# Performance work log

Hardware: AMD Instinct MI355X
Metric: run time of the kernel (lower is better)

## Reference

```python
import jax, jax.numpy as jnp
import numpy as np


def _gru_layer(x, w_ih, w_hh, b_ih, b_hh):
    """PyTorch-semantics GRU over x:[B,T,I]. w_ih:[3H,I], w_hh:[3H,H]."""
    B, T, I = x.shape
    H = w_hh.shape[1]
    # precompute input-side gates for all timesteps: [T,B,3H]
    gx = (jnp.einsum('bti,gi->btg', x, w_ih) + b_ih).transpose(1, 0, 2)

    def step(h, gx_t):
        gh = h @ w_hh.T + b_hh  # [B,3H]
        xr, xz, xn = jnp.split(gx_t, 3, axis=-1)
        hr, hz, hn = jnp.split(gh, 3, axis=-1)
        r = jax.nn.sigmoid(xr + hr)
        z = jax.nn.sigmoid(xz + hz)
        n = jnp.tanh(xn + r * hn)
        h_new = (1.0 - z) * n + z * h
        return h_new, h_new

    h0 = jnp.zeros((B, H), dtype=x.dtype)
    _, hs = jax.lax.scan(step, h0, gx)  # hs: [T,B,H]
    return hs.transpose(1, 0, 2)


def _gru_params(key, in_size, hidden):
    k = 1.0 / np.sqrt(hidden)
    k1, k2, k3, k4 = jax.random.split(key, 4)
    w_ih = jax.random.uniform(k1, (3 * hidden, in_size), minval=-k, maxval=k, dtype=jnp.float32)
    w_hh = jax.random.uniform(k2, (3 * hidden, hidden), minval=-k, maxval=k, dtype=jnp.float32)
    b_ih = jax.random.uniform(k3, (3 * hidden,), minval=-k, maxval=k, dtype=jnp.float32)
    b_hh = jax.random.uniform(k4, (3 * hidden,), minval=-k, maxval=k, dtype=jnp.float32)
    return w_ih, w_hh, b_ih, b_hh


def setup_inputs() -> dict:
    key = jax.random.key(0)
    ks = jax.random.split(key, 6)
    B, T = 256, 1024
    x = jax.random.normal(ks[0], (B, T), dtype=jnp.float32)
    sizes = [(1, 256), (256, 128), (128, 128), (128, 256)]
    d = {'x': x}
    for i, (isz, h) in enumerate(sizes):
        w_ih, w_hh, b_ih, b_hh = _gru_params(ks[1 + i], isz, h)
        d[f'w_ih{i+1}'] = w_ih
        d[f'w_hh{i+1}'] = w_hh
        d[f'b_ih{i+1}'] = b_ih
        d[f'b_hh{i+1}'] = b_hh
    kw, kb = jax.random.split(ks[5])
    kk = 1.0 / np.sqrt(256.0)
    d['w_out'] = jax.random.uniform(kw, (1, 256), minval=-kk, maxval=kk, dtype=jnp.float32)
    d['b_out'] = jax.random.uniform(kb, (1,), minval=-kk, maxval=kk, dtype=jnp.float32)
    return d


def reference(x, w_ih1, w_hh1, b_ih1, b_hh1,
              w_ih2, w_hh2, b_ih2, b_hh2,
              w_ih3, w_hh3, b_ih3, b_hh3,
              w_ih4, w_hh4, b_ih4, b_hh4,
              w_out, b_out):
    h = x[..., None]  # [B,T,1]
    h = _gru_layer(h, w_ih1, w_hh1, b_ih1, b_hh1)
    h = _gru_layer(h, w_ih2, w_hh2, b_ih2, b_hh2)
    h = _gru_layer(h, w_ih3, w_hh3, b_ih3, b_hh3)
    h = _gru_layer(h, w_ih4, w_hh4, b_ih4, b_hh4)
    y = jnp.einsum('bth,oh->bto', h, w_out) + b_out  # TimeDistributed Linear(256,1)
    return y.reshape(y.shape[0], -1)  # flatten from dim 1 -> [B,T]
```

## Files before the change

### kernel.cpp

```cpp
#include <hip/hip_runtime.h>
#include <math.h>


__device__ __forceinline__ float sigmoidf_(float v) {
    return 1.0f / (1.0f + __expf(-v));
}
__device__ __forceinline__ float tanhf_(float v) {
    float e = __expf(2.0f * v);
    return 1.0f - 2.0f / (e + 1.0f);
}

__global__ void prep_k(const float* __restrict__ src, float* __restrict__ dst,
                       int H, int J) {
    int idx = blockIdx.x * 256 + threadIdx.x;
    int total = 3 * H * J;
    if (idx < total) {
        int g = idx / (H * J);
        int rem = idx - g * H * J;
        int u = rem / J;
        int j = rem - u * J;
        dst[(u * 3 + g) * J + j] = src[(g * H + u) * J + j];
    }
}


__device__ __forceinline__ void flag_st(int* p, int v) {
    __hip_atomic_store(p, v, __ATOMIC_RELAXED, __HIP_MEMORY_SCOPE_AGENT);
}
__device__ __forceinline__ int flag_ld(const int* p) {
    return __hip_atomic_load(p, __ATOMIC_RELAXED, __HIP_MEMORY_SCOPE_AGENT);
}
__device__ __forceinline__ void ex_store(float* p, float v) {
    __hip_atomic_store(p, v, __ATOMIC_RELAXED, __HIP_MEMORY_SCOPE_AGENT);
}

__device__ __forceinline__ void pollwait(const int* p, int tgt, bool active,
                                         int& fc) {
    if (threadIdx.x < 64) {
        bool need = active && (fc < tgt);
        if (__any(need)) {
            int spins = 0;
            while (true) {
                if (need) { fc = flag_ld(p); need = (fc < tgt); }
                if (!__any(need)) break;
                if (++spins > 200000) break;
                __builtin_amdgcn_s_sleep(1);
            }
        }
    }
    __syncthreads();
}


template <int J>
__device__ __forceinline__ void stageW(float* dst, const float* src) {
    constexpr int NF4 = J / 32;
    const int lane = threadIdx.x & 63;
    float4 tmp[NF4];
    #pragma unroll
    for (int k = 0; k < NF4; ++k) {
        const float* p = src + (size_t)(k * 64 + lane) * 4;
        asm volatile("global_load_dwordx4 %0, %1, off sc0 sc1"
                     : "=v"(tmp[k]) : "v"(p) : "memory");
    }
    asm volatile("s_waitcnt vmcnt(0)" ::: "memory");
    #pragma unroll
    for (int k = 0; k < NF4; ++k)
        *(float4*)(dst + (k * 64 + lane) * 4) = tmp[k];
}

template <int J>
__device__ __forceinline__ void zeroW(float* dst) {
    const int lane = threadIdx.x & 63;
    #pragma unroll
    for (int k = 0; k < J / 32; ++k)
        *(float4*)(dst + (k * 64 + lane) * 4) = make_float4(0.f, 0.f, 0.f, 0.f);
}

template <int U, int J>
__device__ __forceinline__ void ring_store(float* hout, const float* hst) {
    constexpr int LU = (U == 32) ? 5 : 4;
    #pragma unroll
    for (int k = 0; k < (32 * U) / 256; ++k) {
        int i = k * 256 + threadIdx.x;
        int b = i >> LU;
        int c = i & (U - 1);
        ex_store(hout + b * J + c, hst[b * (U + 4) + c]);
    }
}


template <int J, int WST>
__device__ __forceinline__ void dotA4(const float* __restrict__ wb,
                                      const float* __restrict__ hb, int kl,
                                      float (&a)[8][12]) {
    #pragma unroll 2
    for (int it = 0; it < J / 32; ++it) {
        const int j = (it * 8 + kl) * 4;
        float4 h4[8];
        #pragma unroll
        for (int b = 0; b < 8; ++b)
            h4[b] = *(const float4*)(hb + b * J + j);
        #pragma unroll
        for (int i = 0; i < 4; ++i) {
            #pragma unroll
            for (int ch = 0; ch < 3; ++ch) {
                float4 w = *(const float4*)(wb + i * WST + ch * J + j);
                #pragma unroll
                for (int b8 = 0; b8 < 8; ++b8) {
                    float& acc = a[i * 2 + (b8 >> 2)][ch * 4 + (b8 & 3)];
                    acc = fmaf(w.x, h4[b8].x, acc);
                    acc = fmaf(w.y, h4[b8].y, acc);
                    acc = fmaf(w.z, h4[b8].z, acc);
                    acc = fmaf(w.w, h4[b8].w, acc);
                }
            }
        }
    }
}

template <int J, int WST>
__device__ __forceinline__ void dotB2(const float* __restrict__ wb,
                                      const float* __restrict__ hb, int kl,
                                      float (&a)[8][6]) {
    #pragma unroll 2
    for (int it = 0; it < J / 32; ++it) {
        const int j = (it * 8 + kl) * 4;
        float4 h4[8];
        #pragma unroll
        for (int b = 0; b < 8; ++b)
            h4[b] = *(const float4*)(hb + b * J + j);
        #pragma unroll
        for (int i = 0; i < 2; ++i) {
            #pragma unroll
            for (int ch = 0; ch < 3; ++ch) {
                float4 w = *(const float4*)(wb + i * WST + ch * J + j);
                #pragma unroll
                for (int b8 = 0; b8 < 8; ++b8) {
                    float& acc = a[i * 4 + (b8 >> 1)][ch * 2 + (b8 & 1)];
                    acc = fmaf(w.x, h4[b8].x, acc);
                    acc = fmaf(w.y, h4[b8].y, acc);
                    acc = fmaf(w.z, h4[b8].z, acc);
                    acc = fmaf(w.w, h4[b8].w, acc);
                }
            }
        }
    }
}

template <int G, int F>
__device__ __forceinline__ void rscat(float (&a)[G][F], int kl) {
    #pragma unroll
    for (int lev = 0; (1 << lev) < G; ++lev) {
        const int m = 1 << lev;
        const int g = G >> (lev + 1);
        const bool hi = ((kl >> lev) & 1) != 0;
        #pragma unroll
        for (int gg = 0; gg < g; ++gg) {
            #pragma unroll
            for (int f = 0; f < F; ++f) {
                float give = hi ? a[gg][f] : a[gg + g][f];
                float got = __shfl_xor(give, m, 64);
                a[gg][f] = (hi ? a[gg + g][f] : a[gg][f]) + got;
            }
        }
    }
}

__global__ __launch_bounds__(256) void gru_pipe_kernel(
    const float* __restrict__ x,
    const float* __restrict__ w_ih1,
    const float* __restrict__ b_ih1, const float* __restrict__ b_hh1,
    const float* __restrict__ b_ih2, const float* __restrict__ b_hh2,
    const float* __restrict__ b_ih3, const float* __restrict__ b_hh3,
    const float* __restrict__ b_ih4, const float* __restrict__ b_hh4,
    const float* __restrict__ wA_hh1,
    const float* __restrict__ wA_ih2,
    const float* __restrict__ wA_hh2,
    const float* __restrict__ wA_ih3,
    const float* __restrict__ wA_hh3,
    const float* __restrict__ wA_ih4,
    const float* __restrict__ wA_hh4,
    const float* __restrict__ w_out, const float* __restrict__ b_out,
    int* __restrict__ flags,
    float* __restrict__ ex,
    float* __restrict__ out)
{
    const int tid = threadIdx.x;
    const int lane = tid & 63;
    const int w = tid >> 6;
    const int usl = lane >> 3;
    const int kl = lane & 7;
    const int gf = ((kl & 1) << 2) | (kl & 2) | ((kl >> 2) & 1);
    extern __shared__ float smem[];
    __shared__ float xs[32];

    const int bg = blockIdx.x & 7;
    const int rest = blockIdx.x >> 3;
    const int s = rest >> 3;
    const int us = rest & 7;

    int* fb = flags + bg * 128;
    int* arr_own = fb + s * 32;

    const int* pT = arr_own; int dT = -1000000000; bool aT = false;
    const int* pM = arr_own; bool aM = false;
    if (tid < 8) {
        if (s > 0) { pT = fb + (s - 1) * 32 + tid; dT = 1; aT = true; }
        pM = arr_own + tid; aM = true;
    } else if (tid < 16) {
        if (s < 3) { pT = fb + (s + 1) * 32 + (tid - 8); dT = -3; aT = true; }
    }
    int fcT = 0, fcM = 0;

    float* exb = ex + (size_t)bg * 98304;
    float* h1r = exb;
    float* h2r = exb + 32768;
    float* h3r = exb + 49152;
    float* h4r = exb + 65536;

    if (s == 0) {
        float* wlds = smem;
        float* hprev = smem + 24704;
        float* hst = smem + 32896;
        {
            const float* srcw = wA_hh1 + (size_t)us * 32 * 768;
            for (int i = tid; i < 24576; i += 256) {
                int uu = i / 768, r = i - uu * 768;
                wlds[uu * 772 + r] = srcw[i];
            }
        }
        __syncthreads();
        const int u_sl = usl * 4 + (gf >> 1);
        const int bhi = gf & 1;
        const int u = us * 32 + u_sl;
        const float* wbh = wlds + usl * 4 * 772;
        const float* hbh = hprev + w * 2048;
        const float br = b_ih1[u] + b_hh1[u];
        const float bz = b_ih1[u + 256] + b_hh1[u + 256];
        const float bxn = b_ih1[u + 512];
        const float bhn = b_hh1[u + 512];
        const float wir = w_ih1[u], wiz = w_ih1[u + 256], win = w_ih1[u + 512];
        for (int t = 0; t < 1024; ++t) {
            pollwait(pT, t + dT, aT, fcT);
            if (tid < 32) xs[tid] = x[(size_t)(bg * 32 + tid) * 1024 + t];
            pollwait(pM, t, aM, fcM);
            if (t > 0) stageW<256>(hprev + w * 2048,
                                   h1r + (size_t)((t - 1) & 3) * 8192 + w * 2048);
            else       zeroW<256>(hprev + w * 2048);
            float ah[8][12] = {};
            dotA4<256, 772>(wbh, hbh, kl, ah);
            rscat<8, 12>(ah, kl);
            float* hout = h1r + (size_t)(t & 3) * 8192;
            #pragma unroll
            for (int bl = 0; bl < 4; ++bl) {
                int b32 = w * 8 + bhi * 4 + bl;
                float xv = xs[b32];
                float rr = sigmoidf_(ah[0][bl] + br + xv * wir);
                float zz = sigmoidf_(ah[0][4 + bl] + bz + xv * wiz);
                float nn = tanhf_(xv * win + bxn + rr * (ah[0][8 + bl] + bhn));
                float hp = hprev[b32 * 256 + u];
                hst[b32 * 36 + u_sl] = (1.f - zz) * nn + zz * hp;
            }
            __syncthreads();
            ring_store<32, 256>(hout + us * 32, hst);
            asm volatile("s_waitcnt vmcnt(0)" ::: "memory");
            __syncthreads();
            if (tid == 0) flag_st(arr_own + us, t + 1);
        }
    } else if (s == 1) {
        float* wlds = smem;
        float* hin = smem + 6208;
        float* hprev = smem + 14400;
        float* hst = smem + 18496;
        {
            const float* srcw = wA_hh2 + (size_t)us * 16 * 384;
            for (int i = tid; i < 6144; i += 256) {
                int uu = i / 384, r = i - uu * 384;
                wlds[uu * 388 + r] = srcw[i];
            }
        }
        __syncthreads();
        const int u_sl = usl * 2 + (gf >> 2);
        const int bq = gf & 3;
        const int u = us * 16 + u_sl;
        const float* wbh = wlds + usl * 2 * 388;
        const float* wbi = wA_ih2 + (size_t)(us * 16 + usl * 2) * 768;
        const float* hbi = hin + w * 2048;
        const float* hbh = hprev + w * 1024;
        const float br = b_ih2[u] + b_hh2[u];
        const float bz = b_ih2[u + 128] + b_hh2[u + 128];
        const float bxn = b_ih2[u + 256];
        const float bhn = b_hh2[u + 256];
        for (int t = 0; t < 1024; ++t) {
            pollwait(pT, t + dT, aT, fcT);
            stageW<256>(hin + w * 2048, h1r + (size_t)(t & 3) * 8192 + w * 2048);
            float ai[8][6] = {};
            dotB2<256, 768>(wbi, hbi, kl, ai);
            rscat<8, 6>(ai, kl);
            pollwait(pM, t, aM, fcM);
            if (t > 0) stageW<128>(hprev + w * 1024,
                                   h2r + (size_t)((t - 1) & 3) * 4096 + w * 1024);
            else       zeroW<128>(hprev + w * 1024);
            float ah[8][6] = {};
            dotB2<128, 388>(wbh, hbh, kl, ah);
            rscat<8, 6>(ah, kl);
            float* hout = h2r + (size_t)(t & 3) * 4096;
            #pragma unroll
            for (int bl = 0; bl < 2; ++bl) {
                int b32 = w * 8 + bq * 2 + bl;
                float rr = sigmoidf_(ai[0][bl] + ah[0][bl] + br);
                float zz = sigmoidf_(ai[0][2 + bl] + ah[0][2 + bl] + bz);
                float nn = tanhf_(ai[0][4 + bl] + bxn + rr * (ah[0][4 + bl] + bhn));
                float hp = hprev[b32 * 128 + u];
                hst[b32 * 20 + u_sl] = (1.f - zz) * nn + zz * hp;
            }
            __syncthreads();
            ring_store<16, 128>(hout + us * 16, hst);
            asm volatile("s_waitcnt vmcnt(0)" ::: "memory");
            __syncthreads();
            if (tid == 0) flag_st(arr_own + us, t + 1);
        }
    } else if (s == 2) {
        float* wlds = smem;
        float* hin = smem + 6208;
        float* hprev = smem + 10304;
        float* hst = smem + 14400;
        {
            const float* srcw = wA_hh3 + (size_t)us * 16 * 384;
            for (int i = tid; i < 6144; i += 256) {
                int uu = i / 384, r = i - uu * 384;
                wlds[uu * 388 + r] = srcw[i];
            }
        }
        __syncthreads();
        const int u_sl = usl * 2 + (gf >> 2);
        const int bq = gf & 3;
        const int u = us * 16 + u_sl;
        const float* wbh = wlds + usl * 2 * 388;
        const float* wbi = wA_ih3 + (size_t)(us * 16 + usl * 2) * 384;
        const float* hbi = hin + w * 1024;
        const float* hbh = hprev + w * 1024;
        const float br = b_ih3[u] + b_hh3[u];
        const float bz = b_ih3[u + 128] + b_hh3[u + 128];
        const float bxn = b_ih3[u + 256];
        const float bhn = b_hh3[u + 256];
        for (int t = 0; t < 1024; ++t) {
            pollwait(pT, t + dT, aT, fcT);
            stageW<128>(hin + w * 1024, h2r + (size_t)(t & 3) * 4096 + w * 1024);
            float ai[8][6] = {};
            dotB2<128, 384>(wbi, hbi, kl, ai);
            rscat<8, 6>(ai, kl);
            pollwait(pM, t, aM, fcM);
            if (t > 0) stageW<128>(hprev + w * 1024,
                                   h3r + (size_t)((t - 1) & 3) * 4096 + w * 1024);
            else       zeroW<128>(hprev + w * 1024);
            float ah[8][6] = {};
            dotB2<128, 388>(wbh, hbh, kl, ah);
            rscat<8, 6>(ah, kl);
            float* hout = h3r + (size_t)(t & 3) * 4096;
            #pragma unroll
            for (int bl = 0; bl < 2; ++bl) {
                int b32 = w * 8 + bq * 2 + bl;
                float rr = sigmoidf_(ai[0][bl] + ah[0][bl] + br);
                float zz = sigmoidf_(ai[0][2 + bl] + ah[0][2 + bl] + bz);
                float nn = tanhf_(ai[0][4 + bl] + bxn + rr * (ah[0][4 + bl] + bhn));
                float hp = hprev[b32 * 128 + u];
                hst[b32 * 20 + u_sl] = (1.f - zz) * nn + zz * hp;
            }
            __syncthreads();
            ring_store<16, 128>(hout + us * 16, hst);
            asm volatile("s_waitcnt vmcnt(0)" ::: "memory");
            __syncthreads();
            if (tid == 0) flag_st(arr_own + us, t + 1);
        }
    } else {
        float* wlds = smem;
        float* hin = smem + 24704;
        float* hprev = smem + 28800;
        float* hst = smem + 36992;
        {
            const float* srcw = wA_hh4 + (size_t)us * 32 * 768;
            for (int i = tid; i < 24576; i += 256) {
                int uu = i / 768, r = i - uu * 768;
                wlds[uu * 772 + r] = srcw[i];
            }
        }
        __syncthreads();
        const int u_sl = usl * 4 + (gf >> 1);
        const int bhi = gf & 1;
        const int u = us * 32 + u_sl;
        const float* wbh = wlds + usl * 4 * 772;
        const float* wbi = wA_ih4 + (size_t)(us * 32 + usl * 4) * 384;
        const float* hbi = hin + w * 1024;
        const float* hbh = hprev + w * 2048;
        const float br = b_ih4[u] + b_hh4[u];
        const float bz = b_ih4[u + 256] + b_hh4[u + 256];
        const float bxn = b_ih4[u + 512];
        const float bhn = b_hh4[u + 512];
        const float wo = w_out[u];
        for (int t = 0; t < 1024; ++t) {
            pollwait(pT, t + dT, aT, fcT);
            stageW<128>(hin + w * 1024, h3r + (size_t)(t & 3) * 4096 + w * 1024);
            float ai[8][12] = {};
            dotA4<128, 384>(wbi, hbi, kl, ai);
            rscat<8, 12>(ai, kl);
            pollwait(pM, t, aM, fcM);
            if (t > 0) stageW<256>(hprev + w * 2048,
                                   h4r + (size_t)((t - 1) & 3) * 8192 + w * 2048);
            else       zeroW<256>(hprev + w * 2048);
            float ah[8][12] = {};
            dotA4<256, 772>(wbh, hbh, kl, ah);
            rscat<8, 12>(ah, kl);
            float* hout = h4r + (size_t)(t & 3) * 8192;
            float pk[4];
            #pragma unroll
            for (int bl = 0; bl < 4; ++bl) {
                int b32 = w * 8 + bhi * 4 + bl;
                float rr = sigmoidf_(ai[0][bl] + ah[0][bl] + br);
                float zz = sigmoidf_(ai[0][4 + bl] + ah[0][4 + bl] + bz);
                float nn = tanhf_(ai[0][8 + bl] + bxn + rr * (ah[0][8 + bl] + bhn));
                float hp = hprev[b32 * 256 + u];
                float hnew = (1.f - zz) * nn + zz * hp;
                hst[b32 * 36 + u_sl] = hnew;
                pk[bl] = wo * hnew;
            }
            #pragma unroll
            for (int bl = 0; bl < 4; ++bl) {
                pk[bl] += __shfl_xor(pk[bl], 1, 64);
                pk[bl] += __shfl_xor(pk[bl], 2, 64);
                pk[bl] += __shfl_xor(pk[bl], 8, 64);
                pk[bl] += __shfl_xor(pk[bl], 16, 64);
                pk[bl] += __shfl_xor(pk[bl], 32, 64);
            }
            __syncthreads();
            ring_store<32, 256>(hout + us * 32, hst);
            asm volatile("s_waitcnt vmcnt(0)" ::: "memory");
            __syncthreads();
            if (tid == 0) flag_st(arr_own + us, t + 1);
            if ((lane & 59) == 0) {
                #pragma unroll
                for (int bl = 0; bl < 4; ++bl) {
                    float v = pk[bl];
                    if (us == 0) v += b_out[0];
                    atomicAdd(out + (size_t)(bg * 32 + w * 8 + bhi * 4 + bl) * 1024 + t, v);
                }
            }
        }
    }
}

extern "C" void kernel_launch(void* const* d_in, const int* in_sizes, int n_in,
                              void* d_out, int out_size, void* d_ws, size_t ws_size,
                              hipStream_t stream) {
    const float* x     = (const float*)d_in[0];
    const float* w_ih1 = (const float*)d_in[1];
    const float* w_hh1 = (const float*)d_in[2];
    const float* b_ih1 = (const float*)d_in[3];
    const float* b_hh1 = (const float*)d_in[4];
    const float* w_ih2 = (const float*)d_in[5];
    const float* w_hh2 = (const float*)d_in[6];
    const float* b_ih2 = (const float*)d_in[7];
    const float* b_hh2 = (const float*)d_in[8];
    const float* w_ih3 = (const float*)d_in[9];
    const float* w_hh3 = (const float*)d_in[10];
    const float* b_ih3 = (const float*)d_in[11];
    const float* b_hh3 = (const float*)d_in[12];
    const float* w_ih4 = (const float*)d_in[13];
    const float* w_hh4 = (const float*)d_in[14];
    const float* b_ih4 = (const float*)d_in[15];
    const float* b_hh4 = (const float*)d_in[16];
    const float* w_out = (const float*)d_in[17];
    const float* b_out = (const float*)d_in[18];

    float* ws = (float*)d_ws;
    float* wA_hh1 = ws;
    float* wA_ih2 = wA_hh1 + 196608;
    float* wA_hh2 = wA_ih2 + 98304;
    float* wA_ih3 = wA_hh2 + 49152;
    float* wA_hh3 = wA_ih3 + 49152;
    float* wA_ih4 = wA_hh3 + 49152;
    float* wA_hh4 = wA_ih4 + 98304;
    float* ex     = wA_hh4 + 196608;
    int*   flags  = (int*)(ex + 786432);

    (void)hipMemsetAsync(flags, 0, 1024 * sizeof(int), stream);
    (void)hipMemsetAsync(d_out, 0, 256 * 1024 * sizeof(float), stream);

    prep_k<<<768, 256, 0, stream>>>(w_hh1, wA_hh1, 256, 256);
    prep_k<<<384, 256, 0, stream>>>(w_ih2, wA_ih2, 128, 256);
    prep_k<<<192, 256, 0, stream>>>(w_hh2, wA_hh2, 128, 128);
    prep_k<<<192, 256, 0, stream>>>(w_ih3, wA_ih3, 128, 128);
    prep_k<<<192, 256, 0, stream>>>(w_hh3, wA_hh3, 128, 128);
    prep_k<<<384, 256, 0, stream>>>(w_ih4, wA_ih4, 256, 128);
    prep_k<<<768, 256, 0, stream>>>(w_hh4, wA_hh4, 256, 256);

    const int dyn_lds = 38144 * (int)sizeof(float);
    (void)hipFuncSetAttribute((const void*)gru_pipe_kernel,
                              hipFuncAttributeMaxDynamicSharedMemorySize, dyn_lds);

    gru_pipe_kernel<<<256, 256, dyn_lds, stream>>>(
        x, w_ih1, b_ih1, b_hh1, b_ih2, b_hh2, b_ih3, b_hh3, b_ih4, b_hh4,
        wA_hh1, wA_ih2, wA_hh2, wA_ih3, wA_hh3, wA_ih4, wA_hh4,
        w_out, b_out, flags, ex, (float*)d_out);
}
```

Before: 19.65 ms.

## Split GRU recurrent dot products across two K-halves with 512-thread blocks

Doubles the block to 512 threads and splits each gate dot product's reduction dimension across two wave groups. The partial sums are merged through LDS with an added khmerge step. Input-side and hidden-side gate sums now share one accumulator, the ih2/ih3 weights are staged into LDS, and h is stored directly to the exchange ring instead of via an LDS transpose. The aim is to shorten the per-timestep serial critical path, at the cost of extra __syncthreads and LDS traffic per step and roughly double the register-pressure constraints under launch_bounds(512).

```diff
diff --git a/kernel.cpp b/kernel.cpp
--- a/kernel.cpp
+++ b/kernel.cpp
@@ -53,7 +53,7 @@
 
 
 template <int J>
-__device__ __forceinline__ void stageW(float* dst, const float* src) {
+__device__ __forceinline__ void stage8(float* dst, const float* src) {
     constexpr int NF4 = J / 32;
     const int lane = threadIdx.x & 63;
     float4 tmp[NF4];
@@ -70,90 +70,77 @@
 }
 
 template <int J>
-__device__ __forceinline__ void zeroW(float* dst) {
+__device__ __forceinline__ void zero8(float* dst) {
     const int lane = threadIdx.x & 63;
     #pragma unroll
     for (int k = 0; k < J / 32; ++k)
         *(float4*)(dst + (k * 64 + lane) * 4) = make_float4(0.f, 0.f, 0.f, 0.f);
 }
 
-template <int U, int J>
-__device__ __forceinline__ void ring_store(float* hout, const float* hst) {
-    constexpr int LU = (U == 32) ? 5 : 4;
+template <int J, int WST, int NCH3, int F>
+__device__ __forceinline__ void dotA(const float* __restrict__ wb,
+                                     const float* __restrict__ hb,
+                                     int kh, int kl, float (&a)[8][F]) {
     #pragma unroll
-    for (int k = 0; k < (32 * U) / 256; ++k) {
-        int i = k * 256 + threadIdx.x;
-        int b = i >> LU;
-        int c = i & (U - 1);
-        ex_store(hout + b * J + c, hst[b * (U + 4) + c]);
-    }
-}
-
-
-template <int J, int WST>
-__device__ __forceinline__ void dotA4(const float* __restrict__ wb,
-                                      const float* __restrict__ hb, int kl,
-                                      float (&a)[8][12]) {
-    #pragma unroll 2
-    for (int it = 0; it < J / 32; ++it) {
-        const int j = (it * 8 + kl) * 4;
+    for (int itl = 0; itl < J / 64; ++itl) {
+        const int j = ((kh * (J / 64) + itl) * 8 + kl) * 4;
         float4 h4[8];
         #pragma unroll
-        for (int b = 0; b < 8; ++b)
-            h4[b] = *(const float4*)(hb + b * J + j);
+        for (int b = 0; b < 8; ++b) h4[b] = *(const float4*)(hb + b * J + j);
         #pragma unroll
         for (int i = 0; i < 4; ++i) {
             #pragma unroll
             for (int ch = 0; ch < 3; ++ch) {
-                float4 w = *(const float4*)(wb + i * WST + ch * J + j);
-                #pragma unroll
-                for (int b8 = 0; b8 < 8; ++b8) {
-                    float& acc = a[i * 2 + (b8 >> 2)][ch * 4 + (b8 & 3)];
-                    acc = fmaf(w.x, h4[b8].x, acc);
-                    acc = fmaf(w.y, h4[b8].y, acc);
-                    acc = fmaf(w.z, h4[b8].z, acc);
-                    acc = fmaf(w.w, h4[b8].w, acc);
-                }
-            }
-        }
-    }
-}
-
-template <int J, int WST>
-__device__ __forceinline__ void dotB2(const float* __restrict__ wb,
-                                      const float* __restrict__ hb, int kl,
-                                      float (&a)[8][6]) {
-    #pragma unroll 2
-    for (int it = 0; it < J / 32; ++it) {
-        const int j = (it * 8 + kl) * 4;
+                float4 wv = *(const float4*)(wb + i * 8 * WST + ch * J + j);
+                const int fb = (ch < 2 ? ch : NCH3) * 4;
+                #pragma unroll
+                for (int b = 0; b < 8; ++b) {
+                    float& acc = a[i * 2 + (b >> 2)][fb + (b & 3)];
+                    acc = fmaf(wv.x, h4[b].x, acc);
+                    acc = fmaf(wv.y, h4[b].y, acc);
+                    acc = fmaf(wv.z, h4[b].z, acc);
+                    acc = fmaf(wv.w, h4[b].w, acc);
+                }
+            }
+        }
+    }
+}
+
+template <int J, int WST, int NCH3>
+__device__ __forceinline__ void dotB(const float* __restrict__ wb,
+                                     const float* __restrict__ hb,
+                                     int kh, int kl, float (&a)[8][8]) {
+    #pragma unroll
+    for (int itl = 0; itl < J / 64; ++itl) {
+        const int j = ((kh * (J / 64) + itl) * 8 + kl) * 4;
         float4 h4[8];
         #pragma unroll
-        for (int b = 0; b < 8; ++b)
-            h4[b] = *(const float4*)(hb + b * J + j);
+        for (int b = 0; b < 8; ++b) h4[b] = *(const float4*)(hb + b * J + j);
         #pragma unroll
         for (int i = 0; i < 2; ++i) {
             #pragma unroll
             for (int ch = 0; ch < 3; ++ch) {
-                float4 w = *(const float4*)(wb + i * WST + ch * J + j);
-                #pragma unroll
-                for (int b8 = 0; b8 < 8; ++b8) {
-                    float& acc = a[i * 4 + (b8 >> 1)][ch * 2 + (b8 & 1)];
-                    acc = fmaf(w.x, h4[b8].x, acc);
-                    acc = fmaf(w.y, h4[b8].y, acc);
-                    acc = fmaf(w.z, h4[b8].z, acc);
-                    acc = fmaf(w.w, h4[b8].w, acc);
-                }
-            }
-        }
-    }
-}
-
-template <int G, int F>
-__device__ __forceinline__ void rscat(float (&a)[G][F], int kl) {
+                float4 wv = *(const float4*)(wb + i * 8 * WST + ch * J + j);
+                const int fb = (ch < 2 ? ch : NCH3) * 2;
+                #pragma unroll
+                for (int b = 0; b < 8; ++b) {
+                    float& acc = a[i * 4 + (b >> 1)][fb + (b & 1)];
+                    acc = fmaf(wv.x, h4[b].x, acc);
+                    acc = fmaf(wv.y, h4[b].y, acc);
+                    acc = fmaf(wv.z, h4[b].z, acc);
+                    acc = fmaf(wv.w, h4[b].w, acc);
+                }
+            }
+        }
+    }
+}
+
+template <int F>
+__device__ __forceinline__ void rscat8(float (&a)[8][F], int kl) {
     #pragma unroll
-    for (int lev = 0; (1 << lev) < G; ++lev) {
+    for (int lev = 0; lev < 3; ++lev) {
         const int m = 1 << lev;
-        const int g = G >> (lev + 1);
+        const int g = 8 >> (lev + 1);
         const bool hi = ((kl >> lev) & 1) != 0;
         #pragma unroll
         for (int gg = 0; gg < g; ++gg) {
@@ -167,7 +154,24 @@
     }
 }
 
-__global__ __launch_bounds__(256) void gru_pipe_kernel(
+template <int F, int F0, int NF>
+__device__ __forceinline__ void khmerge(float* xb, float (&a)[8][F],
+                                        int w, int lane) {
+    if (w >= 4) {
+        #pragma unroll
+        for (int k = 0; k < NF; ++k)
+            xb[((w - 4) * 64 + lane) * 8 + k] = a[0][F0 + k];
+    }
+    __syncthreads();
+    if (w < 4) {
+        #pragma unroll
+        for (int k = 0; k < NF; ++k)
+            a[0][F0 + k] += xb[(w * 64 + lane) * 8 + k];
+    }
+    __syncthreads();
+}
+
+__global__ __launch_bounds__(512) void gru_pipe_kernel(
     const float* __restrict__ x,
     const float* __restrict__ w_ih1,
     const float* __restrict__ b_ih1, const float* __restrict__ b_hh1,
@@ -189,9 +193,10 @@
     const int tid = threadIdx.x;
     const int lane = tid & 63;
     const int w = tid >> 6;
+    const int bh = w & 3;
+    const int kh = w >> 2;
     const int usl = lane >> 3;
     const int kl = lane & 7;
-    const int gf = ((kl & 1) << 2) | (kl & 2) | ((kl >> 2) & 1);
     extern __shared__ float smem[];
     __shared__ float xs[32];
 
@@ -200,16 +205,16 @@
     const int s = rest >> 3;
     const int us = rest & 7;
 
-    int* fb = flags + bg * 128;
-    int* arr_own = fb + s * 32;
+    int* fbp = flags + bg * 128;
+    int* arr_own = fbp + s * 32;
 
     const int* pT = arr_own; int dT = -1000000000; bool aT = false;
     const int* pM = arr_own; bool aM = false;
     if (tid < 8) {
-        if (s > 0) { pT = fb + (s - 1) * 32 + tid; dT = 1; aT = true; }
+        if (s > 0) { pT = fbp + (s - 1) * 32 + tid; dT = 1; aT = true; }
         pM = arr_own + tid; aM = true;
     } else if (tid < 16) {
-        if (s < 3) { pT = fb + (s + 1) * 32 + (tid - 8); dT = -3; aT = true; }
+        if (s < 3) { pT = fbp + (s + 1) * 32 + (tid - 8); dT = -3; aT = true; }
     }
     int fcT = 0, fcM = 0;
 
@@ -222,20 +227,21 @@
     if (s == 0) {
         float* wlds = smem;
         float* hprev = smem + 24704;
-        float* hst = smem + 32896;
+        float* xb = smem + 32896;
         {
             const float* srcw = wA_hh1 + (size_t)us * 32 * 768;
-            for (int i = tid; i < 24576; i += 256) {
+            for (int i = tid; i < 24576; i += 512) {
                 int uu = i / 768, r = i - uu * 768;
                 wlds[uu * 772 + r] = srcw[i];
             }
         }
         __syncthreads();
-        const int u_sl = usl * 4 + (gf >> 1);
-        const int bhi = gf & 1;
-        const int u = us * 32 + u_sl;
-        const float* wbh = wlds + usl * 4 * 772;
-        const float* hbh = hprev + w * 2048;
+        const int iown = ((kl & 1) << 1) | ((kl >> 1) & 1);
+        const int k2 = (kl >> 2) & 1;
+        const int ul = usl + 8 * iown;
+        const int u = us * 32 + ul;
+        const float* wbh = wlds + usl * 772;
+        const float* hbh = hprev + bh * 2048;
         const float br = b_ih1[u] + b_hh1[u];
         const float bz = b_ih1[u + 256] + b_hh1[u + 256];
         const float bxn = b_ih1[u + 512];
@@ -245,131 +251,141 @@
             pollwait(pT, t + dT, aT, fcT);
             if (tid < 32) xs[tid] = x[(size_t)(bg * 32 + tid) * 1024 + t];
             pollwait(pM, t, aM, fcM);
-            if (t > 0) stageW<256>(hprev + w * 2048,
-                                   h1r + (size_t)((t - 1) & 3) * 8192 + w * 2048);
-            else       zeroW<256>(hprev + w * 2048);
-            float ah[8][12] = {};
-            dotA4<256, 772>(wbh, hbh, kl, ah);
-            rscat<8, 12>(ah, kl);
-            float* hout = h1r + (size_t)(t & 3) * 8192;
-            #pragma unroll
-            for (int bl = 0; bl < 4; ++bl) {
-                int b32 = w * 8 + bhi * 4 + bl;
-                float xv = xs[b32];
-                float rr = sigmoidf_(ah[0][bl] + br + xv * wir);
-                float zz = sigmoidf_(ah[0][4 + bl] + bz + xv * wiz);
-                float nn = tanhf_(xv * win + bxn + rr * (ah[0][8 + bl] + bhn));
-                float hp = hprev[b32 * 256 + u];
-                hst[b32 * 36 + u_sl] = (1.f - zz) * nn + zz * hp;
-            }
-            __syncthreads();
-            ring_store<32, 256>(hout + us * 32, hst);
+            if (t > 0) stage8<256>(hprev + bh * 2048,
+                                   h1r + (size_t)((t - 1) & 3) * 8192 + bh * 2048);
+            else       zero8<256>(hprev + bh * 2048);
+            float a[8][12] = {};
+            dotA<256, 772, 2, 12>(wbh, hbh, kh, kl, a);
+            rscat8<12>(a, kl);
+            khmerge<12, 0, 8>(xb, a, w, lane);
+            khmerge<12, 8, 4>(xb, a, w, lane);
+            if (w < 4) {
+                float* hout = h1r + (size_t)(t & 3) * 8192;
+                #pragma unroll
+                for (int bl = 0; bl < 4; ++bl) {
+                    int b32 = bh * 8 + k2 * 4 + bl;
+                    float xv = xs[b32];
+                    float rr = sigmoidf_(a[0][bl] + br + xv * wir);
+                    float zz = sigmoidf_(a[0][4 + bl] + bz + xv * wiz);
+                    float nn = tanhf_(xv * win + bxn + rr * (a[0][8 + bl] + bhn));
+                    float hp = hprev[b32 * 256 + u];
+                    ex_store(hout + b32 * 256 + u, (1.f - zz) * nn + zz * hp);
+                }
+            }
             asm volatile("s_waitcnt vmcnt(0)" ::: "memory");
             __syncthreads();
             if (tid == 0) flag_st(arr_own + us, t + 1);
         }
     } else if (s == 1) {
-        float* wlds = smem;
-        float* hin = smem + 6208;
-        float* hprev = smem + 14400;
-        float* hst = smem + 18496;
+        float* whhL = smem;
+        float* wihL = smem + 6208;
+        float* hin = smem + 18560;
+        float* hprev = smem + 26752;
+        float* xb = smem + 30848;
         {
             const float* srcw = wA_hh2 + (size_t)us * 16 * 384;
-            for (int i = tid; i < 6144; i += 256) {
+            for (int i = tid; i < 6144; i += 512) {
                 int uu = i / 384, r = i - uu * 384;
-                wlds[uu * 388 + r] = srcw[i];
+                whhL[uu * 388 + r] = srcw[i];
+            }
+            const float* srci = wA_ih2 + (size_t)us * 16 * 768;
+            for (int i = tid; i < 12288; i += 512) {
+                int uu = i / 768, r = i - uu * 768;
+                wihL[uu * 772 + r] = srci[i];
             }
         }
         __syncthreads();
-        const int u_sl = usl * 2 + (gf >> 2);
-        const int bq = gf & 3;
-        const int u = us * 16 + u_sl;
-        const float* wbh = wlds + usl * 2 * 388;
-        const float* wbi = wA_ih2 + (size_t)(us * 16 + usl * 2) * 768;
-        const float* hbi = hin + w * 2048;
-        const float* hbh = hprev + w * 1024;
+        const int iown = kl & 1;
+        const int bq = (kl & 2) | ((kl >> 2) & 1);
+        const int ul = usl + 8 * iown;
+        const int u = us * 16 + ul;
+        const float* wbi = wihL + usl * 772;
+        const float* wbh = whhL + usl * 388;
         const float br = b_ih2[u] + b_hh2[u];
         const float bz = b_ih2[u + 128] + b_hh2[u + 128];
         const float bxn = b_ih2[u + 256];
         const float bhn = b_hh2[u + 256];
         for (int t = 0; t < 1024; ++t) {
             pollwait(pT, t + dT, aT, fcT);
-            stageW<256>(hin + w * 2048, h1r + (size_t)(t & 3) * 8192 + w * 2048);
-            float ai[8][6] = {};
-            dotB2<256, 768>(wbi, hbi, kl, ai);
-            rscat<8, 6>(ai, kl);
+            stage8<256>(hin + bh * 2048, h1r + (size_t)(t & 3) * 8192 + bh * 2048);
+            float a[8][8] = {};
+            dotB<256, 772, 2>(wbi, hin + bh * 2048, kh, kl, a);
             pollwait(pM, t, aM, fcM);
-            if (t > 0) stageW<128>(hprev + w * 1024,
-                                   h2r + (size_t)((t - 1) & 3) * 4096 + w * 1024);
-            else       zeroW<128>(hprev + w * 1024);
-            float ah[8][6] = {};
-            dotB2<128, 388>(wbh, hbh, kl, ah);
-            rscat<8, 6>(ah, kl);
-            float* hout = h2r + (size_t)(t & 3) * 4096;
-            #pragma unroll
-            for (int bl = 0; bl < 2; ++bl) {
-                int b32 = w * 8 + bq * 2 + bl;
-                float rr = sigmoidf_(ai[0][bl] + ah[0][bl] + br);
-                float zz = sigmoidf_(ai[0][2 + bl] + ah[0][2 + bl] + bz);
-                float nn = tanhf_(ai[0][4 + bl] + bxn + rr * (ah[0][4 + bl] + bhn));
-                float hp = hprev[b32 * 128 + u];
-                hst[b32 * 20 + u_sl] = (1.f - zz) * nn + zz * hp;
-            }
-            __syncthreads();
-            ring_store<16, 128>(hout + us * 16, hst);
+            if (t > 0) stage8<128>(hprev + bh * 1024,
+                                   h2r + (size_t)((t - 1) & 3) * 4096 + bh * 1024);
+            else       zero8<128>(hprev + bh * 1024);
+            dotB<128, 388, 3>(wbh, hprev + bh * 1024, kh, kl, a);
+            rscat8<8>(a, kl);
+            khmerge<8, 0, 8>(xb, a, w, lane);
+            if (w < 4) {
+                float* hout = h2r + (size_t)(t & 3) * 4096;
+                #pragma unroll
+                for (int bl = 0; bl < 2; ++bl) {
+                    int b32 = bh * 8 + bq * 2 + bl;
+                    float rr = sigmoidf_(a[0][bl] + br);
+                    float zz = sigmoidf_(a[0][2 + bl] + bz);
+                    float nn = tanhf_(a[0][4 + bl] + bxn + rr * (a[0][6 + bl] + bhn));
+                    float hp = hprev[b32 * 128 + u];
+                    ex_store(hout + b32 * 128 + u, (1.f - zz) * nn + zz * hp);
+                }
+            }
             asm volatile("s_waitcnt vmcnt(0)" ::: "memory");
             __syncthreads();
             if (tid == 0) flag_st(arr_own + us, t + 1);
         }
     } else if (s == 2) {
-        float* wlds = smem;
-        float* hin = smem + 6208;
-        float* hprev = smem + 10304;
-        float* hst = smem + 14400;
+        float* whhL = smem;
+        float* wihL = smem + 6208;
+        float* hin = smem + 12416;
+        float* hprev = smem + 16512;
+        float* xb = smem + 20608;
         {
             const float* srcw = wA_hh3 + (size_t)us * 16 * 384;
-            for (int i = tid; i < 6144; i += 256) {
+            for (int i = tid; i < 6144; i += 512) {
                 int uu = i / 384, r = i - uu * 384;
-                wlds[uu * 388 + r] = srcw[i];
+                whhL[uu * 388 + r] = srcw[i];
+            }
+            const float* srci = wA_ih3 + (size_t)us * 16 * 384;
+            for (int i = tid; i < 6144; i += 512) {
+                int uu = i / 384, r = i - uu * 384;
+                wihL[uu * 388 + r] = srci[i];
             }
         }
         __syncthreads();
-        const int u_sl = usl * 2 + (gf >> 2);
-        const int bq = gf & 3;
-        const int u = us * 16 + u_sl;
-        const float* wbh = wlds + usl * 2 * 388;
-        const float* wbi = wA_ih3 + (size_t)(us * 16 + usl * 2) * 384;
-        const float* hbi = hin + w * 1024;
-        const float* hbh = hprev + w * 1024;
+        const int iown = kl & 1;
+        const int bq = (kl & 2) | ((kl >> 2) & 1);
+        const int ul = usl + 8 * iown;
+        const int u = us * 16 + ul;
+        const float* wbi = wihL + usl * 388;
+        const float* wbh = whhL + usl * 388;
         const float br = b_ih3[u] + b_hh3[u];
         const float bz = b_ih3[u + 128] + b_hh3[u + 128];
         const float bxn = b_ih3[u + 256];
         const float bhn = b_hh3[u + 256];
         for (int t = 0; t < 1024; ++t) {
             pollwait(pT, t + dT, aT, fcT);
-            stageW<128>(hin + w * 1024, h2r + (size_t)(t & 3) * 4096 + w * 1024);
-            float ai[8][6] = {};
-            dotB2<128, 384>(wbi, hbi, kl, ai);
-            rscat<8, 6>(ai, kl);
+            stage8<128>(hin + bh * 1024, h2r + (size_t)(t & 3) * 4096 + bh * 1024);
+            float a[8][8] = {};
+            dotB<128, 388, 2>(wbi, hin + bh * 1024, kh, kl, a);
             pollwait(pM, t, aM, fcM);
-            if (t > 0) stageW<128>(hprev + w * 1024,
-                                   h3r + (size_t)((t - 1) & 3) * 4096 + w * 1024);
-            else       zeroW<128>(hprev + w * 1024);
-            float ah[8][6] = {};
-            dotB2<128, 388>(wbh, hbh, kl, ah);
-            rscat<8, 6>(ah, kl);
-            float* hout = h3r + (size_t)(t & 3) * 4096;
-            #pragma unroll
-            for (int bl = 0; bl < 2; ++bl) {
-                int b32 = w * 8 + bq * 2 + bl;
-                float rr = sigmoidf_(ai[0][bl] + ah[0][bl] + br);
-                float zz = sigmoidf_(ai[0][2 + bl] + ah[0][2 + bl] + bz);
-                float nn = tanhf_(ai[0][4 + bl] + bxn + rr * (ah[0][4 + bl] + bhn));
-                float hp = hprev[b32 * 128 + u];
-                hst[b32 * 20 + u_sl] = (1.f - zz) * nn + zz * hp;
-            }
-            __syncthreads();
-            ring_store<16, 128>(hout + us * 16, hst);
+            if (t > 0) stage8<128>(hprev + bh * 1024,
+                                   h3r + (size_t)((t - 1) & 3) * 4096 + bh * 1024);
+            else       zero8<128>(hprev + bh * 1024);
+            dotB<128, 388, 3>(wbh, hprev + bh * 1024, kh, kl, a);
+            rscat8<8>(a, kl);
+            khmerge<8, 0, 8>(xb, a, w, lane);
+            if (w < 4) {
+                float* hout = h3r + (size_t)(t & 3) * 4096;
+                #pragma unroll
+                for (int bl = 0; bl < 2; ++bl) {
+                    int b32 = bh * 8 + bq * 2 + bl;
+                    float rr = sigmoidf_(a[0][bl] + br);
+                    float zz = sigmoidf_(a[0][2 + bl] + bz);
+                    float nn = tanhf_(a[0][4 + bl] + bxn + rr * (a[0][6 + bl] + bhn));
+                    float hp = hprev[b32 * 128 + u];
+                    ex_store(hout + b32 * 128 + u, (1.f - zz) * nn + zz * hp);
+                }
+            }
             asm volatile("s_waitcnt vmcnt(0)" ::: "memory");
             __syncthreads();
             if (tid == 0) flag_st(arr_own + us, t + 1);
@@ -378,22 +394,21 @@
         float* wlds = smem;
         float* hin = smem + 24704;
         float* hprev = smem + 28800;
-        float* hst = smem + 36992;
+        float* xb = smem + 36992;
         {
             const float* srcw = wA_hh4 + (size_t)us * 32 * 768;
-            for (int i = tid; i < 24576; i += 256) {
+            for (int i = tid; i < 24576; i += 512) {
                 int uu = i / 768, r = i - uu * 768;
                 wlds[uu * 772 + r] = srcw[i];
             }
         }
         __syncthreads();
-        const int u_sl = usl * 4 + (gf >> 1);
-        const int bhi = gf & 1;
-        const int u = us * 32 + u_sl;
-        const float* wbh = wlds + usl * 4 * 772;
-        const float* wbi = wA_ih4 + (size_t)(us * 32 + usl * 4) * 384;
-        const float* hbi = hin + w * 1024;
-        const float* hbh = hprev + w * 2048;
+        const int iown = ((kl & 1) << 1) | ((kl >> 1) & 1);
+        const int k2 = (kl >> 2) & 1;
+        const int ul = usl + 8 * iown;
+        const int u = us * 32 + ul;
+        const float* wbi = wA_ih4 + (size_t)(us * 32 + usl) * 384;
+        const float* wbh = wlds + usl * 772;
         const float br = b_ih4[u] + b_hh4[u];
         const float bz = b_ih4[u + 256] + b_hh4[u + 256];
         const float bxn = b_ih4[u + 512];
@@ -401,49 +416,50 @@
         const float wo = w_out[u];
         for (int t = 0; t < 1024; ++t) {
             pollwait(pT, t + dT, aT, fcT);
-            stageW<128>(hin + w * 1024, h3r + (size_t)(t & 3) * 4096 + w * 1024);
-            float ai[8][12] = {};
-            dotA4<128, 384>(wbi, hbi, kl, ai);
-            rscat<8, 12>(ai, kl);
+            stage8<128>(hin + bh * 1024, h3r + (size_t)(t & 3) * 4096 + bh * 1024);
+            float a[8][16] = {};
+            dotA<128, 384, 2, 16>(wbi, hin + bh * 1024, kh, kl, a);
             pollwait(pM, t, aM, fcM);
-            if (t > 0) stageW<256>(hprev + w * 2048,
-                                   h4r + (size_t)((t - 1) & 3) * 8192 + w * 2048);
-            else       zeroW<256>(hprev + w * 2048);
-            float ah[8][12] = {};
-            dotA4<256, 772>(wbh, hbh, kl, ah);
-            rscat<8, 12>(ah, kl);
-            float* hout = h4r + (size_t)(t & 3) * 8192;
-            float pk[4];
-            #pragma unroll
-            for (int bl = 0; bl < 4; ++bl) {
-                int b32 = w * 8 + bhi * 4 + bl;
-                float rr = sigmoidf_(ai[0][bl] + ah[0][bl] + br);
-                float zz = sigmoidf_(ai[0][4 + bl] + ah[0][4 + bl] + bz);
-                float nn = tanhf_(ai[0][8 + bl] + bxn + rr * (ah[0][8 + bl] + bhn));
-                float hp = hprev[b32 * 256 + u];
-                float hnew = (1.f - zz) * nn + zz * hp;
-                hst[b32 * 36 + u_sl] = hnew;
-                pk[bl] = wo * hnew;
-            }
-            #pragma unroll
-            for (int bl = 0; bl < 4; ++bl) {
-                pk[bl] += __shfl_xor(pk[bl], 1, 64);
-                pk[bl] += __shfl_xor(pk[bl], 2, 64);
-                pk[bl] += __shfl_xor(pk[bl], 8, 64);
-                pk[bl] += __shfl_xor(pk[bl], 16, 64);
-                pk[bl] += __shfl_xor(pk[bl], 32, 64);
-            }
-            __syncthreads();
-            ring_store<32, 256>(hout + us * 32, hst);
+            if (t > 0) stage8<256>(hprev + bh * 2048,
+                                   h4r + (size_t)((t - 1) & 3) * 8192 + bh * 2048);
+            else       zero8<256>(hprev + bh * 2048);
+            dotA<256, 772, 3, 16>(wbh, hprev + bh * 2048, kh, kl, a);
+            rscat8<16>(a, kl);
+            khmerge<16, 0, 8>(xb, a, w, lane);
+            khmerge<16, 8, 8>(xb, a, w, lane);
+            float pk[4] = {0.f, 0.f, 0.f, 0.f};
+            if (w < 4) {
+                float* hout = h4r + (size_t)(t & 3) * 8192;
+                #pragma unroll
+                for (int bl = 0; bl < 4; ++bl) {
+                    int b32 = bh * 8 + k2 * 4 + bl;
+                    float rr = sigmoidf_(a[0][bl] + br);
+                    float zz = sigmoidf_(a[0][4 + bl] + bz);
+                    float nn = tanhf_(a[0][8 + bl] + bxn + rr * (a[0][12 + bl] + bhn));
+                    float hp = hprev[b32 * 256 + u];
+                    float hnew = (1.f - zz) * nn + zz * hp;
+                    ex_store(hout + b32 * 256 + u, hnew);
+                    pk[bl] = wo * hnew;
+                }
+                #pragma unroll
+                for (int bl = 0; bl < 4; ++bl) {
+                    pk[bl] += __shfl_xor(pk[bl], 1, 64);
+                    pk[bl] += __shfl_xor(pk[bl], 2, 64);
+                    pk[bl] += __shfl_xor(pk[bl], 8, 64);
+                    pk[bl] += __shfl_xor(pk[bl], 16, 64);
+                    pk[bl] += __shfl_xor(pk[bl], 32, 64);
+                }
+            }
             asm volatile("s_waitcnt vmcnt(0)" ::: "memory");
             __syncthreads();
             if (tid == 0) flag_st(arr_own + us, t + 1);
-            if ((lane & 59) == 0) {
+            if (w < 4 && (lane & 59) == 0) {
                 #pragma unroll
                 for (int bl = 0; bl < 4; ++bl) {
                     float v = pk[bl];
                     if (us == 0) v += b_out[0];
-                    atomicAdd(out + (size_t)(bg * 32 + w * 8 + bhi * 4 + bl) * 1024 + t, v);
+                    atomicAdd(out + (size_t)(bg * 32 + bh * 8 +
+                              ((lane >> 2) & 1) * 4 + bl) * 1024 + t, v);
                 }
             }
         }
@@ -495,11 +511,11 @@
     prep_k<<<384, 256, 0, stream>>>(w_ih4, wA_ih4, 256, 128);
     prep_k<<<768, 256, 0, stream>>>(w_hh4, wA_hh4, 256, 256);
 
-    const int dyn_lds = 38144 * (int)sizeof(float);
+    const int dyn_lds = 39040 * (int)sizeof(float);
     (void)hipFuncSetAttribute((const void*)gru_pipe_kernel,
                               hipFuncAttributeMaxDynamicSharedMemorySize, dyn_lds);
 
-    gru_pipe_kernel<<<256, 256, dyn_lds, stream>>>(
+    gru_pipe_kernel<<<256, 512, dyn_lds, stream>>>(
         x, w_ih1, b_ih1, b_hh1, b_ih2, b_hh2, b_ih3, b_hh3, b_ih4, b_hh4,
         wA_hh1, wA_ih2, wA_hh2, wA_ih3, wA_hh3, wA_ih4, wA_hh4,
         w_out, b_out, flags, ex, (float*)d_out);
```

Result: slower. 20.78 ms (+5.7%).
